# Kernel tuning notes

Measured on AMD Instinct MI355X. Metric: run time of the kernel, lower is better.

Reference implementation:

```python
import jax, jax.numpy as jnp
import numpy as np

N_HEAD = 16
SPARSE_TOPK = 64
NEG_INF = float('-inf')


def setup_inputs() -> dict:
    key = jax.random.key(0)
    ks = jax.random.split(key, 12)
    B, T, C = 4, 1024, 1024
    s = 0.02
    q = jax.random.normal(ks[0], (B, T, C), jnp.float32)
    kv = jax.random.normal(ks[1], (B, T, C), jnp.float32)  # forward asserts k == v
    tgt_mask = jnp.tril(jnp.ones((T, T), jnp.bool_)).reshape(1, 1, T, T)
    inp = {'q': q, 'k': kv, 'v': kv, 'tgt_mask': tgt_mask}
    for i, n in enumerate(['Wq', 'Wk', 'Wv', 'Wo']):
        inp[n] = jax.random.normal(ks[2 + i], (C, C), jnp.float32) * s
    for i, n in enumerate(['bq', 'bk', 'bv', 'bo']):
        inp[n] = jax.random.normal(ks[6 + i], (C,), jnp.float32) * s
    return inp


def reference(q, k, v, tgt_mask, Wq, Wk, Wv, Wo, bq, bk, bv, bo):
    B, T, C = q.shape
    H = N_HEAD
    hd = C // H
    scale = 1.0 / np.sqrt(hd).astype(np.float32)
    # QKV projections -> [B, H, T, hd]
    qh = (q @ Wq + bq).reshape(B, T, H, hd).transpose(0, 2, 1, 3)
    kh = (k @ Wk + bk).reshape(B, T, H, hd).transpose(0, 2, 1, 3)
    vh = (v @ Wv + bv).reshape(B, T, H, hd).transpose(0, 2, 1, 3)
    # full attention scores [B, H, T, T]
    att = jnp.einsum('bhtd,bhsd->bhts', qh, kh) * scale
    # causal mask: masked_fill where tgt_mask == 0
    att = jnp.where(tgt_mask[:, :, :T, :T], att, NEG_INF)
    # top-k sparse pruning: keep entries >= k-th largest per row (ties kept)
    top, _ = jax.lax.top_k(att, SPARSE_TOPK)
    vk = top[..., -1:]  # [B, H, T, 1]
    att = jnp.where(att < vk, NEG_INF, att)
    att = jax.nn.softmax(att, axis=-1)
    # dropout is identity in eval (p=0.0)
    y = jnp.einsum('bhts,bhsd->bhtd', att, vh)
    y = y.transpose(0, 2, 1, 3).reshape(B, T, C)
    return y @ Wo + bo
```

## Files before the change

kernel.cpp:

```cpp
#include <hip/hip_runtime.h>
#include <hip/hip_bf16.h>
#include <math.h>

typedef __attribute__((ext_vector_type(8))) short short8;
typedef __attribute__((ext_vector_type(4))) float f32x4;
typedef __attribute__((ext_vector_type(4))) int int4v;

#define SCL 0.1803368801111204f

static __device__ __forceinline__ unsigned short f2bf(float f) {
  unsigned u = __float_as_uint(f);
  u = u + 0x7FFFu + ((u >> 16) & 1u);
  return (unsigned short)(u >> 16);
}

static __device__ __forceinline__ unsigned keyof(float x) {
  unsigned u = __float_as_uint(x);
  return (u & 0x80000000u) ? ~u : (u | 0x80000000u);
}
static __device__ __forceinline__ float keyinv(unsigned k) {
  unsigned u = (k & 0x80000000u) ? (k & 0x7FFFFFFFu) : ~k;
  return __uint_as_float(u);
}

#define DPP_RED_STEP(x, OP, CTRL) \
  x = OP(x, __int_as_float(__builtin_amdgcn_mov_dpp(__float_as_int(x), CTRL, 0xf, 0xf, true)))
static __device__ __forceinline__ void red_maxmin(float& mx, float& mn) {
  DPP_RED_STEP(mx, fmaxf, 0xB1); DPP_RED_STEP(mn, fminf, 0xB1);
  DPP_RED_STEP(mx, fmaxf, 0x4E); DPP_RED_STEP(mn, fminf, 0x4E);
  DPP_RED_STEP(mx, fmaxf, 0x141); DPP_RED_STEP(mn, fminf, 0x141);
  DPP_RED_STEP(mx, fmaxf, 0x140); DPP_RED_STEP(mn, fminf, 0x140);
  mx = fmaxf(mx, __shfl_xor(mx, 16)); mn = fminf(mn, __shfl_xor(mn, 16));
  mx = fmaxf(mx, __shfl_xor(mx, 32)); mn = fminf(mn, __shfl_xor(mn, 32));
}
#undef DPP_RED_STEP
static __device__ __forceinline__ float red_sum2(float s) {
#define DPP_ADD(x, CTRL) \
  x = x + __int_as_float(__builtin_amdgcn_mov_dpp(__float_as_int(x), CTRL, 0xf, 0xf, true))
  DPP_ADD(s, 0xB1); DPP_ADD(s, 0x4E); DPP_ADD(s, 0x141); DPP_ADD(s, 0x140);
#undef DPP_ADD
  s += __shfl_xor(s, 16);
  s += __shfl_xor(s, 32);
  return s;
}

static __device__ __forceinline__ int saddr(int r, int c) {
  return ((r << 12) + (c << 2)) ^ ((r & 7) << 4);
}
static __device__ __forceinline__ int paddr(int r, int c) {
  return ((r << 12) + (c << 1)) ^ ((r & 7) << 4);
}

static __device__ __forceinline__ void gld_lds16(const unsigned short* g, unsigned short* l) {
  __builtin_amdgcn_global_load_lds(
      (const __attribute__((address_space(1))) void*)g,
      (__attribute__((address_space(3))) void*)l, 16, 0, 0);
}

__global__ __launch_bounds__(256) void cvt3_k(const float* __restrict__ q,
                                              const float* __restrict__ k,
                                              const float* __restrict__ v,
                                              unsigned short* __restrict__ oq,
                                              unsigned short* __restrict__ ok,
                                              unsigned short* __restrict__ ov) {
  const int y = blockIdx.y;
  const float* in = (y == 0) ? q : (y == 1) ? k : v;
  unsigned short* out = (y == 0) ? oq : (y == 1) ? ok : ov;
  const int i = blockIdx.x * 256 + threadIdx.x;
  const f32x4* p = (const f32x4*)in + 2 * (size_t)i;
  f32x4 a = p[0], b = p[1];
  short8 r;
  r[0] = (short)f2bf(a[0]); r[1] = (short)f2bf(a[1]);
  r[2] = (short)f2bf(a[2]); r[3] = (short)f2bf(a[3]);
  r[4] = (short)f2bf(b[0]); r[5] = (short)f2bf(b[1]);
  r[6] = (short)f2bf(b[2]); r[7] = (short)f2bf(b[3]);
  ((short8*)out)[i] = r;
}

__global__ __launch_bounds__(256) void wtrans4_k(const float* __restrict__ Wq,
                                                 const float* __restrict__ Wk,
                                                 const float* __restrict__ Wv,
                                                 const float* __restrict__ Wo,
                                                 unsigned short* __restrict__ Wqt,
                                                 unsigned short* __restrict__ Wkt,
                                                 unsigned short* __restrict__ Wvt,
                                                 unsigned short* __restrict__ Wot) {
  const int z = blockIdx.z;
  const float* W = (z == 0) ? Wq : (z == 1) ? Wk : (z == 2) ? Wv : Wo;
  unsigned short* Wt = (z == 0) ? Wqt : (z == 1) ? Wkt : (z == 2) ? Wvt : Wot;
  __shared__ float tile[32][33];
  const int tx = threadIdx.x, ty = threadIdx.y;
  const int x0 = blockIdx.x * 32, y0 = blockIdx.y * 32;
#pragma unroll
  for (int j = 0; j < 4; ++j)
    tile[ty + j * 8][tx] = W[(y0 + ty + j * 8) * 1024 + x0 + tx];
  __syncthreads();
#pragma unroll
  for (int j = 0; j < 4; ++j)
    Wt[(x0 + ty + j * 8) * 1024 + (y0 + tx)] = f2bf(tile[tx][ty + j * 8]);
}

template <int MODE>
static __device__ __forceinline__ void gemm_body(unsigned short* As0, unsigned short* Bs0,
                                                 unsigned short* As1, unsigned short* Bs1,
                                                 const unsigned short* __restrict__ A,
                                                 const unsigned short* __restrict__ Bt,
                                                 const float* __restrict__ bias,
                                                 void* __restrict__ out) {
  const int tid = threadIdx.x;
  const int lane = tid & 63, w = tid >> 6;
  const int wr = w >> 1, wc = w & 1;
  const int m0 = blockIdx.y * 128, n0 = blockIdx.x * 128;
  const int l15 = lane & 15, l4 = lane >> 4;
  f32x4 acc[4][4] = {};
  const int r0 = tid >> 2, s0 = (tid & 3) * 8;
  const int r1 = r0 + 64;
  const unsigned short* gA0 = A + (m0 + r0) * 1024 + s0;
  const unsigned short* gA1 = A + (m0 + r1) * 1024 + s0;
  const unsigned short* gB0 = Bt + (n0 + r0) * 1024 + s0;
  const unsigned short* gB1 = Bt + (n0 + r1) * 1024 + s0;
  const int oA0 = r0 * 32 + s0, oA1 = r1 * 32 + s0;

  gld_lds16(gA0, As0 + oA0);
  gld_lds16(gA1, As0 + oA1);
  gld_lds16(gB0, Bs0 + oA0);
  gld_lds16(gB1, Bs0 + oA1);
  __syncthreads();

  for (int kt = 0; kt < 32; ++kt) {
    if (kt < 31) {
      const int k0n = (kt + 1) * 32;
      unsigned short* Asn = (kt & 1) ? As0 : As1;
      unsigned short* Bsn = (kt & 1) ? Bs0 : Bs1;
      gld_lds16(gA0 + k0n, Asn + oA0);
      gld_lds16(gA1 + k0n, Asn + oA1);
      gld_lds16(gB0 + k0n, Bsn + oA0);
      gld_lds16(gB1 + k0n, Bsn + oA1);
    }
    const unsigned short* Asc = (kt & 1) ? As1 : As0;
    const unsigned short* Bsc = (kt & 1) ? Bs1 : Bs0;
    short8 af[4], bfr[4];
#pragma unroll
    for (int i = 0; i < 4; ++i) {
      af[i]  = *(const short8*)(Asc + (wr * 64 + i * 16 + l15) * 32 + l4 * 8);
      bfr[i] = *(const short8*)(Bsc + (wc * 64 + i * 16 + l15) * 32 + l4 * 8);
    }
#pragma unroll
    for (int i = 0; i < 4; ++i)
#pragma unroll
      for (int j = 0; j < 4; ++j)
        acc[i][j] = __builtin_amdgcn_mfma_f32_16x16x32_bf16(af[i], bfr[j], acc[i][j], 0, 0, 0);
    __syncthreads();
  }
#pragma unroll
  for (int i = 0; i < 4; ++i) {
#pragma unroll
    for (int j = 0; j < 4; ++j) {
      const int n = n0 + wc * 64 + j * 16 + l15;
      const float bv = bias[n];
#pragma unroll
      for (int r = 0; r < 4; ++r) {
        const int m = m0 + wr * 64 + i * 16 + l4 * 4 + r;
        const float v = acc[i][j][r] + bv;
        if (MODE == 2) {
          ((float*)out)[m * 1024 + n] = v;
        } else {
          const int bb = m >> 10, t = m & 1023, hh = n >> 6, dd = n & 63;
          const unsigned short bfv = f2bf(v);
          if (MODE == 0)
            ((unsigned short*)out)[(((bb << 4) + hh) * 1024 + t) * 64 + dd] = bfv;
          else
            ((unsigned short*)out)[(((bb << 4) + hh) * 64 + dd) * 1024 + t] = bfv;
        }
      }
    }
  }
}

__global__ __launch_bounds__(256) void gemm_qkv_k(
    const unsigned short* qbf, const unsigned short* kbf, const unsigned short* vbf,
    const unsigned short* Wqt, const unsigned short* Wkt, const unsigned short* Wvt,
    const float* bq, const float* bk, const float* bv,
    unsigned short* Qh, unsigned short* Kh, unsigned short* Vth) {
  __shared__ unsigned short As0[128 * 32], Bs0[128 * 32], As1[128 * 32], Bs1[128 * 32];
  const int z = blockIdx.z;
  const unsigned short* A  = (z == 0) ? qbf : ((z == 1) ? kbf : vbf);
  const unsigned short* Bt = (z == 0) ? Wqt : ((z == 1) ? Wkt : Wvt);
  const float* bias        = (z == 0) ? bq  : ((z == 1) ? bk  : bv);
  if (z == 2) gemm_body<1>(As0, Bs0, As1, Bs1, A, Bt, bias, Vth);
  else        gemm_body<0>(As0, Bs0, As1, Bs1, A, Bt, bias, z ? Kh : Qh);
}

__global__ __launch_bounds__(256) void gemm_out_k(const unsigned short* Y,
                                                  const unsigned short* Wot,
                                                  const float* bo, float* out) {
  __shared__ unsigned short As0[128 * 32], Bs0[128 * 32], As1[128 * 32], Bs1[128 * 32];
  gemm_body<2>(As0, Bs0, As1, Bs1, Y, Wot, bo, out);
}

__global__ __launch_bounds__(1024, 8) void attn_k(const unsigned short* __restrict__ Q,
                                                  const unsigned short* __restrict__ K,
                                                  const unsigned short* __restrict__ Vt,
                                                  unsigned short* __restrict__ Y) {
  extern __shared__ __align__(16) char smem[];
  const int tid = threadIdx.x, lane = tid & 63, w = tid >> 6;
  const int bid = (int)blockIdx.x;
  const int wk = (bid & 7) * 512 + (bid >> 3);
  const int hp = wk >> 6;
  const int tc = wk & 63;
  const int t0 = 1008 - 16 * tc;
  const int b = hp >> 4, h = hp & 15;
  const unsigned short* Qp = Q + (((b * 16 + h) * 1024) + t0) * 64;
  const unsigned short* Kh = K + (b * 16 + h) * 65536;
  const unsigned short* Vh = Vt + (b * 16 + h) * 65536;
  const int L = t0 + 16;
  const int Lpad = (L + 31) & ~31;
  const int nCT = L >> 4;
  const bool full = (L > 512);
  const int l15 = lane & 15, l4 = lane >> 4;
  float* RED3 = (float*)(smem + 65536);
  float* RED2 = (float*)(smem + 65536 + 13056);

  const short8 aq0 = *(const short8*)(Qp + l15 * 64 + l4 * 8);
  const short8 aq1 = *(const short8*)(Qp + l15 * 64 + 32 + l4 * 8);

  for (int ct = w; ct < nCT; ct += 16) {
    const int c0 = ct * 16;
    const short8 kb0 = *(const short8*)(Kh + (c0 + l15) * 64 + l4 * 8);
    const short8 kb1 = *(const short8*)(Kh + (c0 + l15) * 64 + 32 + l4 * 8);
    f32x4 acc = {0.f, 0.f, 0.f, 0.f};
    __builtin_amdgcn_s_setprio(1);
    acc = __builtin_amdgcn_mfma_f32_16x16x32_bf16(aq0, kb0, acc, 0, 0, 0);
    acc = __builtin_amdgcn_mfma_f32_16x16x32_bf16(aq1, kb1, acc, 0, 0, 0);
    __builtin_amdgcn_s_setprio(0);
    const int c = c0 + l15;
    if (ct == nCT - 1) {
#pragma unroll
      for (int r = 0; r < 4; ++r) {
        const int row = l4 * 4 + r;
        *(float*)(smem + saddr(row, c)) = (c <= t0 + row) ? acc[r] * SCL : -INFINITY;
      }
    } else {
#pragma unroll
      for (int r = 0; r < 4; ++r)
        *(float*)(smem + saddr(l4 * 4 + r, c)) = acc[r] * SCL;
    }
  }
  __syncthreads();

  const int Lr = t0 + w + 1;
  float v[16];
#pragma unroll
  for (int p = 0; p < 8; ++p) {
    const int c = (p << 7) + (lane << 1);
    const float2 t = *(const float2*)(smem + saddr(w, c));
    const bool vld = c < L;
    v[2 * p]     = vld ? t.x : -INFINITY;
    v[2 * p + 1] = vld ? t.y : -INFINITY;
  }

  float lm = v[0];
#pragma unroll
  for (int i = 1; i < 16; ++i) lm = fmaxf(lm, v[i]);
  float mx = lm, mn = lm;
  red_maxmin(mx, mn);

  auto countge = [&](float tm) {
    int cnt = 0;
#pragma unroll
    for (int i = 0; i < 8; ++i) cnt += (int)__popcll(__ballot(v[i] >= tm));
    if (full) {
#pragma unroll
      for (int i = 8; i < 16; ++i) cnt += (int)__popcll(__ballot(v[i] >= tm));
    }
    return cnt;
  };

  float thr = -INFINITY;
  if (Lr > 64) {
    unsigned lo = (unsigned)__builtin_amdgcn_readfirstlane((int)keyof(mn));
    unsigned hi = (unsigned)__builtin_amdgcn_readfirstlane((int)keyof(mx)) + 1u;
    int cl = Lr, ch = 0, alt = 0;
    for (int it = 0; it < 64 && (hi - lo) > 1u; ++it) {
      const unsigned span = hi - lo;
      unsigned off;
      if (alt) off = span >> 1;
      else {
        const float fr = (float)(cl - 64) / (float)(cl - ch);
        off = (unsigned)(fr * (float)span);
        if (off < 1u) off = 1u;
        if (off > span - 1u) off = span - 1u;
      }
      alt ^= 1;
      const unsigned mid = lo + off;
      const int cnt = countge(keyinv(mid));
      if (cnt >= 64) { lo = mid; cl = cnt; if (cnt == 64) hi = mid + 1u; }
      else { hi = mid; ch = cnt; }
    }
    thr = keyinv(lo);
  }

  float s = 0.f;
  unsigned pk[8];
#pragma unroll
  for (int p = 0; p < 4; ++p) {
    const float p0 = (v[2 * p]     >= thr) ? exp2f(v[2 * p]     - mx) : 0.f;
    const float p1 = (v[2 * p + 1] >= thr) ? exp2f(v[2 * p + 1] - mx) : 0.f;
    s += p0 + p1;
    pk[p] = (unsigned)f2bf(p0) | ((unsigned)f2bf(p1) << 16);
  }
  if (full) {
#pragma unroll
    for (int p = 4; p < 8; ++p) {
      const float p0 = (v[2 * p]     >= thr) ? exp2f(v[2 * p]     - mx) : 0.f;
      const float p1 = (v[2 * p + 1] >= thr) ? exp2f(v[2 * p + 1] - mx) : 0.f;
      s += p0 + p1;
      pk[p] = (unsigned)f2bf(p0) | ((unsigned)f2bf(p1) << 16);
    }
  }
#pragma unroll
  for (int p = 0; p < 4; ++p) {
    const int c = (p << 7) + (lane << 1);
    if (c < Lpad) *(unsigned*)(smem + paddr(w, c)) = pk[p];
  }
  if (full) {
#pragma unroll
    for (int p = 4; p < 8; ++p) {
      const int c = ((p & 3) << 7) + (lane << 1) + 512;
      if (c < Lpad) *(unsigned*)(smem + paddr(w, c)) = pk[p];
    }
  }
  s = red_sum2(s);
  if (lane == 0) RED2[w] = 1.f / s;
  __syncthreads();

  const int nST = Lpad >> 5;
  const int qd = (nST + 3) >> 2;
  const int kseg = w >> 2;
  const int d0 = (w & 3) * 16;
  int klo = kseg * qd, khi = klo + qd;
  if (klo > nST) klo = nST;
  if (khi > nST) khi = nST;
  f32x4 acc = {0.f, 0.f, 0.f, 0.f};
  for (int st = klo; st < khi; ++st) {
    const int sb = st * 32 + l4 * 8;
    const short8 paf = *(const short8*)(smem + paddr(l15, sb));
    const short8 vb = *(const short8*)(Vh + (d0 + l15) * 1024 + sb);
    __builtin_amdgcn_s_setprio(1);
    acc = __builtin_amdgcn_mfma_f32_16x16x32_bf16(paf, vb, acc, 0, 0, 0);
    __builtin_amdgcn_s_setprio(0);
  }
  if (kseg > 0) {
#pragma unroll
    for (int r = 0; r < 4; ++r)
      RED3[((kseg - 1) * 16 + l4 * 4 + r) * 68 + d0 + l15] = acc[r];
  }
  __syncthreads();
  if (kseg == 0) {
    const int d = (h << 6) + d0 + l15;
#pragma unroll
    for (int r = 0; r < 4; ++r) {
      const int row = l4 * 4 + r;
      const int col = d0 + l15;
      float sv = acc[r] + RED3[row * 68 + col] + RED3[(16 + row) * 68 + col] +
                 RED3[(32 + row) * 68 + col];
      Y[((b << 10) + t0 + row) * 1024 + d] = f2bf(sv * RED2[row]);
    }
  }
}

extern "C" void kernel_launch(void* const* d_in, const int* in_sizes, int n_in,
                              void* d_out, int out_size, void* d_ws, size_t ws_size,
                              hipStream_t stream) {
  const float* q  = (const float*)d_in[0];
  const float* k  = (const float*)d_in[1];
  const float* v  = (const float*)d_in[2];
  const float* Wq = (const float*)d_in[4];
  const float* Wk = (const float*)d_in[5];
  const float* Wv = (const float*)d_in[6];
  const float* Wo = (const float*)d_in[7];
  const float* bq = (const float*)d_in[8];
  const float* bk = (const float*)d_in[9];
  const float* bv = (const float*)d_in[10];
  const float* bo = (const float*)d_in[11];

  char* ws = (char*)d_ws;
  const size_t MB = 1u << 20;
  unsigned short* qbf = (unsigned short*)(ws + 0 * MB);
  unsigned short* kbf = (unsigned short*)(ws + 8 * MB);
  unsigned short* vbf = (unsigned short*)(ws + 16 * MB);
  unsigned short* Wqt = (unsigned short*)(ws + 24 * MB);
  unsigned short* Wkt = (unsigned short*)(ws + 26 * MB);
  unsigned short* Wvt = (unsigned short*)(ws + 28 * MB);
  unsigned short* Wot = (unsigned short*)(ws + 30 * MB);
  unsigned short* Qh  = (unsigned short*)(ws + 32 * MB);
  unsigned short* Kh  = (unsigned short*)(ws + 40 * MB);
  unsigned short* Vth = (unsigned short*)(ws + 48 * MB);
  unsigned short* Y   = qbf;

  cvt3_k<<<dim3(2048, 3), 256, 0, stream>>>(q, k, v, qbf, kbf, vbf);
  wtrans4_k<<<dim3(32, 32, 4), dim3(32, 8), 0, stream>>>(Wq, Wk, Wv, Wo, Wqt, Wkt, Wvt, Wot);
  gemm_qkv_k<<<dim3(8, 32, 3), 256, 0, stream>>>(qbf, kbf, vbf, Wqt, Wkt, Wvt,
                                                 bq, bk, bv, Qh, Kh, Vth);
  attn_k<<<dim3(4096), 1024, 78656, stream>>>(Qh, Kh, Vth, Y);
  gemm_out_k<<<dim3(8, 32), 256, 0, stream>>>(Y, Wot, bo, (float*)d_out);
}
```

Baseline: 209.6 us.

## Remap GEMM blocks per XCD, precompute LDS addresses, use raw v_exp_f32

The QKV and output GEMMs switch to a 1D grid whose block index is decoded so that blocks sharing the same A row-tiles land on the same XCD, which is meant to improve L2 reuse of the activations. The attention kernel replaces the per-access saddr/paddr swizzle calls with precomputed base offsets. It also replaces exp2f with inline v_exp_f32 asm to skip range-handling code. The raw exp instruction handles denormals differently, and the hardcoded swizzle must match the original address functions exactly.

```diff
diff --git a/kernel.cpp b/kernel.cpp
--- a/kernel.cpp
+++ b/kernel.cpp
@@ -12,6 +12,12 @@
   unsigned u = __float_as_uint(f);
   u = u + 0x7FFFu + ((u >> 16) & 1u);
   return (unsigned short)(u >> 16);
+}
+
+static __device__ __forceinline__ float fexp2(float x) {
+  float r;
+  asm("v_exp_f32 %0, %1" : "=v"(r) : "v"(x));
+  return r;
 }
 
 static __device__ __forceinline__ unsigned keyof(float x) {
@@ -106,11 +112,11 @@
                                                  const unsigned short* __restrict__ A,
                                                  const unsigned short* __restrict__ Bt,
                                                  const float* __restrict__ bias,
-                                                 void* __restrict__ out) {
+                                                 void* __restrict__ out,
+                                                 const int m0, const int n0) {
   const int tid = threadIdx.x;
   const int lane = tid & 63, w = tid >> 6;
   const int wr = w >> 1, wc = w & 1;
-  const int m0 = blockIdx.y * 128, n0 = blockIdx.x * 128;
   const int l15 = lane & 15, l4 = lane >> 4;
   f32x4 acc[4][4] = {};
   const int r0 = tid >> 2, s0 = (tid & 3) * 8;
@@ -183,19 +189,28 @@
     const float* bq, const float* bk, const float* bv,
     unsigned short* Qh, unsigned short* Kh, unsigned short* Vth) {
   __shared__ unsigned short As0[128 * 32], Bs0[128 * 32], As1[128 * 32], Bs1[128 * 32];
-  const int z = blockIdx.z;
+  const int bid = (int)blockIdx.x;
+  const int xcd = bid & 7, idx = bid >> 3;
+  const int z = idx >> 5;
+  const int rem = idx & 31;
+  const int m0 = (xcd * 4 + (rem >> 3)) * 128;
+  const int n0 = (rem & 7) * 128;
   const unsigned short* A  = (z == 0) ? qbf : ((z == 1) ? kbf : vbf);
   const unsigned short* Bt = (z == 0) ? Wqt : ((z == 1) ? Wkt : Wvt);
   const float* bias        = (z == 0) ? bq  : ((z == 1) ? bk  : bv);
-  if (z == 2) gemm_body<1>(As0, Bs0, As1, Bs1, A, Bt, bias, Vth);
-  else        gemm_body<0>(As0, Bs0, As1, Bs1, A, Bt, bias, z ? Kh : Qh);
+  if (z == 2) gemm_body<1>(As0, Bs0, As1, Bs1, A, Bt, bias, Vth, m0, n0);
+  else        gemm_body<0>(As0, Bs0, As1, Bs1, A, Bt, bias, z ? Kh : Qh, m0, n0);
 }
 
 __global__ __launch_bounds__(256) void gemm_out_k(const unsigned short* Y,
                                                   const unsigned short* Wot,
                                                   const float* bo, float* out) {
   __shared__ unsigned short As0[128 * 32], Bs0[128 * 32], As1[128 * 32], Bs1[128 * 32];
-  gemm_body<2>(As0, Bs0, As1, Bs1, Y, Wot, bo, out);
+  const int bid = (int)blockIdx.x;
+  const int xcd = bid & 7, idx = bid >> 3;
+  const int m0 = (xcd * 4 + (idx >> 3)) * 128;
+  const int n0 = (idx & 7) * 128;
+  gemm_body<2>(As0, Bs0, As1, Bs1, Y, Wot, bo, out, m0, n0);
 }
 
 __global__ __launch_bounds__(1024, 8) void attn_k(const unsigned short* __restrict__ Q,
@@ -249,11 +264,12 @@
   __syncthreads();
 
   const int Lr = t0 + w + 1;
+  const int sbase = (w << 12) | ((lane << 3) ^ ((w & 7) << 4));
   float v[16];
 #pragma unroll
   for (int p = 0; p < 8; ++p) {
     const int c = (p << 7) + (lane << 1);
-    const float2 t = *(const float2*)(smem + saddr(w, c));
+    const float2 t = *(const float2*)(smem + sbase + (p << 9));
     const bool vld = c < L;
     v[2 * p]     = vld ? t.x : -INFINITY;
     v[2 * p + 1] = vld ? t.y : -INFINITY;
@@ -300,20 +316,21 @@
     thr = keyinv(lo);
   }
 
+  const int pbase = (w << 12) | ((lane << 2) ^ ((w & 7) << 4));
   float s = 0.f;
   unsigned pk[8];
 #pragma unroll
   for (int p = 0; p < 4; ++p) {
-    const float p0 = (v[2 * p]     >= thr) ? exp2f(v[2 * p]     - mx) : 0.f;
-    const float p1 = (v[2 * p + 1] >= thr) ? exp2f(v[2 * p + 1] - mx) : 0.f;
+    const float p0 = (v[2 * p]     >= thr) ? fexp2(v[2 * p]     - mx) : 0.f;
+    const float p1 = (v[2 * p + 1] >= thr) ? fexp2(v[2 * p + 1] - mx) : 0.f;
     s += p0 + p1;
     pk[p] = (unsigned)f2bf(p0) | ((unsigned)f2bf(p1) << 16);
   }
   if (full) {
 #pragma unroll
     for (int p = 4; p < 8; ++p) {
-      const float p0 = (v[2 * p]     >= thr) ? exp2f(v[2 * p]     - mx) : 0.f;
-      const float p1 = (v[2 * p + 1] >= thr) ? exp2f(v[2 * p + 1] - mx) : 0.f;
+      const float p0 = (v[2 * p]     >= thr) ? fexp2(v[2 * p]     - mx) : 0.f;
+      const float p1 = (v[2 * p + 1] >= thr) ? fexp2(v[2 * p + 1] - mx) : 0.f;
       s += p0 + p1;
       pk[p] = (unsigned)f2bf(p0) | ((unsigned)f2bf(p1) << 16);
     }
@@ -321,13 +338,13 @@
 #pragma unroll
   for (int p = 0; p < 4; ++p) {
     const int c = (p << 7) + (lane << 1);
-    if (c < Lpad) *(unsigned*)(smem + paddr(w, c)) = pk[p];
+    if (c < Lpad) *(unsigned*)(smem + pbase + (p << 8)) = pk[p];
   }
   if (full) {
 #pragma unroll
     for (int p = 4; p < 8; ++p) {
       const int c = ((p & 3) << 7) + (lane << 1) + 512;
-      if (c < Lpad) *(unsigned*)(smem + paddr(w, c)) = pk[p];
+      if (c < Lpad) *(unsigned*)(smem + pbase + ((p & 3) << 8) + 1024) = pk[p];
     }
   }
   s = red_sum2(s);
@@ -400,8 +417,8 @@
 
   cvt3_k<<<dim3(2048, 3), 256, 0, stream>>>(q, k, v, qbf, kbf, vbf);
   wtrans4_k<<<dim3(32, 32, 4), dim3(32, 8), 0, stream>>>(Wq, Wk, Wv, Wo, Wqt, Wkt, Wvt, Wot);
-  gemm_qkv_k<<<dim3(8, 32, 3), 256, 0, stream>>>(qbf, kbf, vbf, Wqt, Wkt, Wvt,
-                                                 bq, bk, bv, Qh, Kh, Vth);
+  gemm_qkv_k<<<dim3(768), 256, 0, stream>>>(qbf, kbf, vbf, Wqt, Wkt, Wvt,
+                                            bq, bk, bv, Qh, Kh, Vth);
   attn_k<<<dim3(4096), 1024, 78656, stream>>>(Qh, Kh, Vth, Y);
-  gemm_out_k<<<dim3(8, 32), 256, 0, stream>>>(Y, Wot, bo, (float*)d_out);
-}
+  gemm_out_k<<<dim3(256), 256, 0, stream>>>(Y, Wot, bo, (float*)d_out);
+}
```

New measurement: 202.4 us, median of 2. 3.5% less time.
